# Optimization experiments

Hardware: AMD Instinct MI355X
Metric: run time of the kernel (lower is better)

## Reference

```python
import jax, jax.numpy as jnp
import numpy as np

NUM_HEADS = 4
KEY_DIM = 128


def rel_to_abs(rel):
    # rel: [B, heads, L, ww, 2*ww-1] -> [B, heads, L, ww, ww]
    B, heads, L, ww, dim = rel.shape
    flat = rel.reshape(B, heads, L, ww * (2 * ww - 1))[:, :, :, ww - 1:-1]
    return flat.reshape(B, heads, L, ww, 2 * (ww - 1))[..., :ww]


def relative_logits(pos_q, pos_emb_w, pos_emb_h):
    # pos_q: [B, hh, ww, heads, kd]
    # width logits
    q_w = jnp.transpose(pos_q, (0, 3, 1, 2, 4))           # [B, heads, hh, ww, kd]
    rel_w = jnp.einsum('bhxyd,dr->bhxyr', q_w, pos_emb_w)  # [B, heads, hh, ww, 2ww-1]
    rel_w = rel_to_abs(rel_w)                              # [B, heads, hh, ww, ww]
    # height logits
    q_h = jnp.transpose(pos_q, (0, 3, 2, 1, 4))           # [B, heads, ww, hh, kd]
    rel_h = jnp.einsum('bhyxd,dr->bhyxr', q_h, pos_emb_h)  # [B, heads, ww, hh, 2hh-1]
    rel_h = rel_to_abs(rel_h)                              # [B, heads, ww, hh, hh]
    rel_h = jnp.transpose(rel_h, (0, 1, 3, 2, 4))          # [B, heads, hh, ww, hh]
    # broadcast-add: [B, heads, hh, ww, hh, ww]
    return rel_w[:, :, :, :, None, :] + rel_h[:, :, :, :, :, None]


def setup_inputs() -> dict:
    key = jax.random.key(0)
    ks = jax.random.split(key, 7)
    B, H, W, C = 8, 32, 32, 512
    emb = NUM_HEADS * KEY_DIM
    stddev = KEY_DIM ** (-0.5)
    return {
        'x': jax.random.normal(ks[0], (B, H, W, C), jnp.float32),
        'Wq': jax.random.normal(ks[1], (C, emb), jnp.float32) * 0.02,
        'Wk': jax.random.normal(ks[2], (C, emb), jnp.float32) * 0.02,
        'Wv': jax.random.normal(ks[3], (C, emb), jnp.float32) * 0.02,
        'Wo': jax.random.normal(ks[4], (emb, emb), jnp.float32) * 0.02,
        'pos_emb_w': jax.random.normal(ks[5], (KEY_DIM, 2 * W - 1), jnp.float32) * stddev,
        'pos_emb_h': jax.random.normal(ks[6], (KEY_DIM, 2 * H - 1), jnp.float32) * stddev,
    }


def reference(x, Wq, Wk, Wv, Wo, pos_emb_w, pos_emb_h):
    B, hh, ww, C = x.shape
    heads, kd = NUM_HEADS, KEY_DIM
    L = hh * ww
    scale = 1.0 / jnp.sqrt(jnp.asarray(kd, x.dtype))

    q = (x @ Wq) * scale                                    # [B, hh, ww, heads*kd]
    attn_q = q.reshape(B, L, heads, kd).transpose(0, 2, 1, 3)   # [B, heads, L, kd]
    pos_q = q.reshape(B, hh, ww, heads, kd)
    k = (x @ Wk).reshape(B, L, heads, kd).transpose(0, 2, 3, 1)  # [B, heads, kd, L]
    v = (x @ Wv).reshape(B, L, heads, kd).transpose(0, 2, 1, 3)  # [B, heads, L, kd]

    scores = attn_q @ k                                      # [B, heads, L, L]
    pos = relative_logits(pos_q, pos_emb_w, pos_emb_h)        # [B, heads, hh, ww, hh, ww]
    scores = scores + pos.reshape(B, heads, L, L)
    attn = jax.nn.softmax(scores, axis=-1)

    out = attn @ v                                            # [B, heads, L, kd]
    out = out.transpose(0, 2, 1, 3).reshape(B, hh, ww, heads * kd)
    return out @ Wo
```

## Files before the change

kernel.cpp:

```cpp
#include <hip/hip_runtime.h>
#include <math.h>

typedef unsigned short u16;
typedef unsigned int u32;
typedef __bf16 bf16x8 __attribute__((ext_vector_type(8)));
typedef float f32x4 __attribute__((ext_vector_type(4)));

__device__ __forceinline__ u16 f2b(float f) {
  u32 u = __builtin_bit_cast(u32, f);
  u32 r = (u + 0x7FFFu + ((u >> 16) & 1u)) >> 16;
  return (u16)r;
}

__device__ __forceinline__ void glds16(const void* g, void* lds) {
  __builtin_amdgcn_global_load_lds(
      (const __attribute__((address_space(1))) void*)(void*)(const_cast<void*>(g)),
      (__attribute__((address_space(3))) void*)lds, 16, 0, 0);
}

#define QSCALE (0.08838834764831845f * 1.4426950408889634f)


__global__ __launch_bounds__(256) void castx(const float* __restrict__ x, u16* __restrict__ xb) {
  int idx = blockIdx.x * 256 + threadIdx.x;
  float4 v = ((const float4*)x)[idx];
  ushort4 o;
  o.x = f2b(v.x); o.y = f2b(v.y); o.z = f2b(v.z); o.w = f2b(v.w);
  ((ushort4*)xb)[idx] = o;
}

__global__ __launch_bounds__(256) void buildw(const float* __restrict__ Wq, const float* __restrict__ Wk,
                                              const float* __restrict__ Wv, const float* __restrict__ Wo,
                                              u16* __restrict__ WbigT, u16* __restrict__ WoT) {
  int row = blockIdx.x;
  int t = threadIdx.x;
  if (row < 512) {
    for (int k = t; k < 512; k += 256) WbigT[row*512 + k] = f2b(Wq[k*512 + row] * QSCALE);
  } else if (row < 1024) {
    int n = row - 512;
    for (int k = t; k < 512; k += 256) WbigT[row*512 + k] = f2b(Wk[k*512 + n]);
  } else if (row < 1536) {
    int n = row - 1024;
    for (int k = t; k < 512; k += 256) WbigT[row*512 + k] = f2b(Wv[k*512 + n]);
  } else if (row < 1544) {
    int rr = row - 1536 + 2040;
    for (int k = t; k < 512; k += 256) WbigT[rr*512 + k] = 0;
  } else {
    int n = row - 1544;
    for (int k = t; k < 512; k += 256) WoT[n*512 + k] = f2b(Wo[k*512 + n]);
  }
}

__global__ __launch_bounds__(256) void wpe_kernel(const float* __restrict__ Wq, const float* __restrict__ pew,
                                                  const float* __restrict__ peh, u16* __restrict__ WbigT) {
  int k = blockIdx.x;
  int t = threadIdx.x;
  __shared__ float wrow[512];
  for (int j = t; j < 512; j += 256) wrow[j] = Wq[k*512 + j];
  __syncthreads();
  if (t < 252) {
    int h = t / 63, r = t - h*63;
    float aw = 0.f, ah = 0.f;
    for (int d = 0; d < 128; d++) {
      float qv = wrow[h*128 + d];
      aw += qv * pew[d*63 + r];
      ah += qv * peh[d*63 + r];
    }
    WbigT[(size_t)(1536 + t)*512 + k] = f2b(aw * QSCALE);
    WbigT[(size_t)(1788 + t)*512 + k] = f2b(ah * QSCALE);
  }
}

__global__ __launch_bounds__(512) void gemm256(
    const u16* __restrict__ A, const u16* __restrict__ Bt,
    u16* __restrict__ Qb, u16* __restrict__ Kb, u16* __restrict__ Vt,
    float* __restrict__ RELW, float* __restrict__ RELH)
{
  __shared__ char sm[131072];
  const int tid = threadIdx.x;
  const int w = tid >> 6, l = tid & 63, g = l >> 4, c = l & 15;
  const int bm = blockIdx.x, bn = blockIdx.y;
  const int wm = w >> 2, wn = w & 3;

  f32x4 acc[8][4];
#pragma unroll
  for (int i = 0; i < 8; i++)
#pragma unroll
    for (int j = 0; j < 4; j++) acc[i][j] = f32x4{0.f, 0.f, 0.f, 0.f};

  const char* Ab = (const char*)A;
  const char* Bb = (const char*)Bt;
  const int rsub = l >> 3;
  const int csw = (((l & 7) ^ rsub) << 4);

#define A_STAGE(kb, p)                                                                    \
  {                                                                                       \
    char* As_ = sm + (p)*65536;                                                           \
    const int kbyte = (kb) * 128;                                                         \
    _Pragma("unroll")                                                                     \
    for (int i2 = 0; i2 < 4; i2++) {                                                      \
      const int row = i2*64 + w*8 + rsub;                                                 \
      glds16(Ab + (size_t)(bm*256 + row) * 1024 + kbyte + csw, As_ + i2*8192 + w*1024);   \
    }                                                                                     \
  }
#define B_STAGE(kb, p)                                                                    \
  {                                                                                       \
    char* Bs_ = sm + (p)*65536 + 32768;                                                   \
    const int kbyte = (kb) * 128;                                                         \
    _Pragma("unroll")                                                                     \
    for (int i2 = 0; i2 < 4; i2++) {                                                      \
      const int row = i2*64 + w*8 + rsub;                                                 \
      glds16(Bb + (size_t)(bn*256 + row) * 1024 + kbyte + csw, Bs_ + i2*8192 + w*1024);   \
    }                                                                                     \
  }

  B_STAGE(0, 0); A_STAGE(0, 0);
  B_STAGE(1, 1); A_STAGE(1, 1);

#pragma unroll
  for (int kb = 0; kb < 8; kb++) {
    const int p = kb & 1;
    if (kb == 0)      { asm volatile("s_waitcnt vmcnt(8)" ::: "memory"); }
    else if (kb < 7)  { asm volatile("s_waitcnt vmcnt(4)" ::: "memory"); }
    else              { asm volatile("s_waitcnt vmcnt(0)" ::: "memory"); }
    __builtin_amdgcn_s_barrier();

    const char* As_ = sm + p*65536;
    const char* Bs_ = As_ + 32768;

    bf16x8 bf[4][2], af[4][2];
#pragma unroll
    for (int ks = 0; ks < 2; ks++) {
      const int koff = (ks*64 + g*16) ^ ((c & 7) << 4);
#pragma unroll
      for (int mf = 0; mf < 4; mf++)
        af[mf][ks] = *(const bf16x8*)(As_ + (wm*128 + mf*16 + c)*128 + koff);
#pragma unroll
      for (int nf = 0; nf < 4; nf++)
        bf[nf][ks] = *(const bf16x8*)(Bs_ + (wn*64 + nf*16 + c)*128 + koff);
    }
    if (kb >= 1 && kb < 7) A_STAGE(kb + 1, p ^ 1);
    __builtin_amdgcn_s_setprio(1);
#pragma unroll
    for (int ks = 0; ks < 2; ks++)
#pragma unroll
      for (int mf = 0; mf < 4; mf++)
#pragma unroll
        for (int nf = 0; nf < 4; nf++)
          acc[mf][nf] = __builtin_amdgcn_mfma_f32_16x16x32_bf16(af[mf][ks], bf[nf][ks], acc[mf][nf], 0, 0, 0);
    __builtin_amdgcn_s_setprio(0);
    __builtin_amdgcn_s_barrier();

#pragma unroll
    for (int ks = 0; ks < 2; ks++) {
      const int koff = (ks*64 + g*16) ^ ((c & 7) << 4);
#pragma unroll
      for (int mf = 0; mf < 4; mf++)
        af[mf][ks] = *(const bf16x8*)(As_ + (wm*128 + (mf + 4)*16 + c)*128 + koff);
    }
    if (kb < 6) B_STAGE(kb + 2, p);
    __builtin_amdgcn_s_setprio(1);
#pragma unroll
    for (int ks = 0; ks < 2; ks++)
#pragma unroll
      for (int mf = 0; mf < 4; mf++)
#pragma unroll
        for (int nf = 0; nf < 4; nf++)
          acc[mf + 4][nf] = __builtin_amdgcn_mfma_f32_16x16x32_bf16(af[mf][ks], bf[nf][ks], acc[mf + 4][nf], 0, 0, 0);
    __builtin_amdgcn_s_setprio(0);
    __builtin_amdgcn_s_barrier();
  }
#undef A_STAGE
#undef B_STAGE

  const int b = bm >> 2;
  const int iBase = (bm & 3) * 256;

  if (bn < 4) {
    u16* dst0 = (bn < 2) ? Qb : Kb;
    const int bnn = bn & 1;
#pragma unroll
    for (int mf = 0; mf < 8; mf++) {
      const int lmb = wm*128 + mf*16 + g*4;
#pragma unroll
      for (int nf = 0; nf < 4; nf++) {
        const int ln = wn*64 + nf*16 + c;
#pragma unroll
        for (int r = 0; r < 4; r++) {
          const int lm = lmb + r;
          *(u16*)(sm + lm*512 + ((ln*2) ^ ((lm & 7) << 4))) = f2b(acc[mf][nf][r]);
        }
      }
    }
    __builtin_amdgcn_s_barrier();
#pragma unroll
    for (int it = 0; it < 16; it++) {
      const int gid = it*512 + tid;
      const int lm2 = gid >> 5, gsub = gid & 31;
      bf16x8 v = *(const bf16x8*)(sm + lm2*512 + ((gsub*16) ^ ((lm2 & 7) << 4)));
      const int h = bnn*2 + (gsub >> 4);
      const int d0 = (gsub & 15) * 8;
      *(bf16x8*)(dst0 + ((size_t)(b*4 + h)*1024 + iBase + lm2)*128 + d0) = v;
    }
  } else if (bn < 6) {
#pragma unroll
    for (int mf = 0; mf < 8; mf++) {
      const int lmb = wm*128 + mf*16 + g*4;
#pragma unroll
      for (int nf = 0; nf < 4; nf++) {
        const int ln = wn*64 + nf*16 + c;
        u32 w0, w1;
        asm("v_cvt_pk_bf16_f32 %0, %1, %2" : "=v"(w0) : "v"(acc[mf][nf][0]), "v"(acc[mf][nf][1]));
        asm("v_cvt_pk_bf16_f32 %0, %1, %2" : "=v"(w1) : "v"(acc[mf][nf][2]), "v"(acc[mf][nf][3]));
        uint2 pk; pk.x = w0; pk.y = w1;
        *(uint2*)(sm + ln*512 + ((lmb*2) ^ ((c & 7) << 4))) = pk;
      }
    }
    __builtin_amdgcn_s_barrier();
#pragma unroll
    for (int it = 0; it < 16; it++) {
      const int gid = it*512 + tid;
      const int ln2 = gid >> 5, gsub = gid & 31;
      bf16x8 v = *(const bf16x8*)(sm + ln2*512 + ((gsub*16) ^ ((ln2 & 7) << 4)));
      const int q2 = (bn - 4)*256 + ln2;
      const int h = q2 >> 7, d = q2 & 127;
      *(bf16x8*)(Vt + ((size_t)(b*4 + h)*128 + d)*1024 + iBase + gsub*8) = v;
    }
  } else {
#pragma unroll
    for (int mf = 0; mf < 8; mf++) {
      const int lmb = wm*128 + mf*16 + g*4;
#pragma unroll
      for (int nf = 0; nf < 4; nf++) {
        const int q = (bn - 6)*256 + wn*64 + nf*16 + c;
        if (q < 252) {
          const int h = q / 63, r2 = q - h*63;
#pragma unroll
          for (int r = 0; r < 4; r++)
            RELW[(size_t)((b*4 + h)*1024 + iBase + lmb + r)*64 + r2] = acc[mf][nf][r];
        } else if (q < 504) {
          const int qq = q - 252;
          const int h = qq / 63, r2 = qq - h*63;
#pragma unroll
          for (int r = 0; r < 4; r++)
            RELH[(size_t)((b*4 + h)*1024 + iBase + lmb + r)*64 + r2] = acc[mf][nf][r];
        }
      }
    }
  }
}

__global__ __launch_bounds__(256) void attn_fused(
    const u16* __restrict__ Qb, const u16* __restrict__ Kb, const u16* __restrict__ Vt,
    const float* __restrict__ RELW, const float* __restrict__ RELH,
    u16* __restrict__ AO)
{
  __shared__ char sm[73728];
  char* const Pl = sm + 65536;
  const int tid = threadIdx.x;
  const int w = tid >> 6, l = tid & 63, g = l >> 4, c = l & 15;
  const int bh = blockIdx.x, qt = blockIdx.y;
  const int i0 = qt * 64;

  bf16x8 qf[4];
  {
    const char* qbase = (const char*)Qb + (size_t)(bh*1024 + i0 + w*16 + c) * 256;
#pragma unroll
    for (int s = 0; s < 4; s++) qf[s] = *(const bf16x8*)(qbase + s*64 + g*16);
  }

  const int i = i0 + w*16 + c;
  const int xi = i & 31, yi = i >> 5;
  const float* rw = RELW + ((size_t)(bh*1024 + i) << 6);
  const float* rhb = RELH + ((size_t)(bh*1024 + i) << 6) + (31 - yi);
  float xwh[2][4];
#pragma unroll
  for (int e = 0; e < 2; e++)
#pragma unroll
    for (int r = 0; r < 4; r++) xwh[e][r] = rw[e*16 + g*4 + r - xi + 31];

  f32x4 Oacc[8];
#pragma unroll
  for (int fd = 0; fd < 8; fd++) Oacc[fd] = f32x4{0.f, 0.f, 0.f, 0.f};
  float m_q = -INFINITY, l_q = 0.f;

#define A_STAGE(jt, p)                                                                     \
  {                                                                                        \
    char* Kt_ = sm + (p)*32768;                                                            \
    char* Vs_ = Kt_ + 16384;                                                               \
    const int j0b = (jt) * 64;                                                             \
    _Pragma("unroll")                                                                      \
    for (int t = 0; t < 4; t++) {                                                          \
      const int L = (w*4 + t)*1024 + l*16;                                                 \
      const int jr = L >> 8, jb = L & 255;                                                 \
      glds16((const char*)Kb + (size_t)(bh*1024 + j0b + jr) * 256 + (jb ^ ((jr & 7) << 4)),\
             Kt_ + L);                                                                     \
      const int dr = L >> 7, db = L & 127;                                                 \
      glds16((const char*)Vt + (size_t)(bh*128 + dr) * 2048 + j0b*2 + (db ^ ((dr & 7) << 4)),\
             Vs_ + L);                                                                     \
    }                                                                                      \
  }

  A_STAGE(0, 0);
  A_STAGE(1, 1);
  float yh0 = rhb[0], yh1 = rhb[1];

#pragma unroll 2
  for (int jt = 0; jt < 16; jt++) {
    const int p = jt & 1;
    if (jt < 15) { asm volatile("s_waitcnt vmcnt(8)" ::: "memory"); }
    else         { asm volatile("s_waitcnt vmcnt(0)" ::: "memory"); }
    __builtin_amdgcn_s_barrier();

    const char* Kt_ = sm + p*32768;
    const char* Vs_ = Kt_ + 16384;

    f32x4 acc[4];
#pragma unroll
    for (int fn = 0; fn < 4; fn++) acc[fn] = f32x4{0.f, 0.f, 0.f, 0.f};
    __builtin_amdgcn_s_setprio(1);
#pragma unroll
    for (int s = 0; s < 4; s++) {
      const int koff = (s*64 + g*16) ^ ((c & 7) << 4);
#pragma unroll
      for (int fn = 0; fn < 4; fn++) {
        bf16x8 kf = *(const bf16x8*)(Kt_ + (fn*16 + c)*256 + koff);
        acc[fn] = __builtin_amdgcn_mfma_f32_16x16x32_bf16(kf, qf[s], acc[fn], 0, 0, 0);
      }
    }
    __builtin_amdgcn_s_setprio(0);

#pragma unroll
    for (int fn = 0; fn < 4; fn++)
#pragma unroll
      for (int r = 0; r < 4; r++)
        acc[fn][r] += xwh[fn & 1][r] + ((fn >> 1) ? yh1 : yh0);

    float mx = fmaxf(fmaxf(fmaxf(acc[0][0], acc[0][1]), fmaxf(acc[0][2], acc[0][3])),
                     fmaxf(fmaxf(acc[1][0], acc[1][1]), fmaxf(acc[1][2], acc[1][3])));
    mx = fmaxf(mx, fmaxf(fmaxf(fmaxf(acc[2][0], acc[2][1]), fmaxf(acc[2][2], acc[2][3])),
                         fmaxf(fmaxf(acc[3][0], acc[3][1]), fmaxf(acc[3][2], acc[3][3]))));
    mx = fmaxf(mx, __shfl_xor(mx, 16));
    mx = fmaxf(mx, __shfl_xor(mx, 32));

    if (__any(mx > m_q + 8.f)) {
      const float mnew = fmaxf(m_q, mx);
      const float scq = exp2f(m_q - mnew);
      m_q = mnew;
      l_q *= scq;
#pragma unroll
      for (int r = 0; r < 4; r++) {
        const float scr = __shfl(scq, g*4 + r, 16);
#pragma unroll
        for (int fd = 0; fd < 8; fd++) Oacc[fd][r] *= scr;
      }
    }

    float pv[4][4];
    float ps = 0.f;
#pragma unroll
    for (int fn = 0; fn < 4; fn++) {
#pragma unroll
      for (int r = 0; r < 4; r++) {
        pv[fn][r] = exp2f(acc[fn][r] - m_q);
        ps += pv[fn][r];
      }
    }
    ps += __shfl_xor(ps, 16);
    ps += __shfl_xor(ps, 32);
    l_q += ps;

    float nyh0 = 0.f, nyh1 = 0.f;
    if (jt < 15) { nyh0 = rhb[(jt + 1)*2]; nyh1 = rhb[(jt + 1)*2 + 1]; }

    {
      char* pb = Pl + w*2048 + c*128;
      const int swz = (c & 7) << 4;
#pragma unroll
      for (int fn = 0; fn < 4; fn++) {
        u32 w0, w1;
        asm("v_cvt_pk_bf16_f32 %0, %1, %2" : "=v"(w0) : "v"(pv[fn][0]), "v"(pv[fn][1]));
        asm("v_cvt_pk_bf16_f32 %0, %1, %2" : "=v"(w1) : "v"(pv[fn][2]), "v"(pv[fn][3]));
        uint2 pk; pk.x = w0; pk.y = w1;
        *(uint2*)(pb + ((fn*32 + g*8) ^ swz)) = pk;
      }
    }

    __builtin_amdgcn_s_setprio(1);
#pragma unroll
    for (int s = 0; s < 2; s++) {
      const int koff = (s*64 + g*16) ^ ((c & 7) << 4);
      bf16x8 pf = *(const bf16x8*)(Pl + w*2048 + c*128 + koff);
#pragma unroll
      for (int fd = 0; fd < 8; fd++) {
        bf16x8 vf = *(const bf16x8*)(Vs_ + (fd*16 + c)*128 + koff);
        Oacc[fd] = __builtin_amdgcn_mfma_f32_16x16x32_bf16(pf, vf, Oacc[fd], 0, 0, 0);
      }
    }
    __builtin_amdgcn_s_setprio(0);

    __builtin_amdgcn_s_barrier();
    if (jt < 14) A_STAGE(jt + 2, p);
    yh0 = nyh0; yh1 = nyh1;
  }

  const int b = bh >> 2, h = bh & 3;
#pragma unroll
  for (int r = 0; r < 4; r++) {
    const float lr = __shfl(l_q, g*4 + r, 16);
    const float linv = 1.0f / lr;
    const int io = i0 + w*16 + g*4 + r;
#pragma unroll
    for (int fd = 0; fd < 8; fd++) {
      AO[(size_t)(b*1024 + io)*512 + h*128 + fd*16 + c] = f2b(Oacc[fd][r] * linv);
    }
  }
#undef A_STAGE
}

__global__ __launch_bounds__(256) void gemm_out(
    const u16* __restrict__ A, const u16* __restrict__ Bt, float* __restrict__ outF)
{
  __shared__ char sm[65536];
  const int tid = threadIdx.x;
  const int w = tid >> 6, l = tid & 63, g = l >> 4, c = l & 15;
  const int bm = blockIdx.x, bn = blockIdx.y;
  const int wm = (w >> 1) * 64, wn = (w & 1) * 64;

  f32x4 acc[4][4];
#pragma unroll
  for (int i = 0; i < 4; i++)
#pragma unroll
    for (int j = 0; j < 4; j++) acc[i][j] = f32x4{0.f, 0.f, 0.f, 0.f};

  const char* Ab = (const char*)A;
  const char* Bb = (const char*)Bt;
  const int rsub = l >> 3;
  const int csw = (((l & 7) ^ rsub) << 4);

#define G_STAGE(kb, p)                                                                    \
  {                                                                                       \
    char* As_ = sm + (p)*32768;                                                           \
    char* Bs_ = As_ + 16384;                                                              \
    const int kbyte = (kb) * 128;                                                         \
    _Pragma("unroll")                                                                     \
    for (int t = 0; t < 4; t++) {                                                         \
      const int row = (w*4 + t)*8 + rsub;                                                 \
      glds16(Ab + (size_t)(bm*128 + row) * 1024 + kbyte + csw, As_ + (w*4 + t)*1024);     \
      glds16(Bb + (size_t)(bn*128 + row) * 1024 + kbyte + csw, Bs_ + (w*4 + t)*1024);     \
    }                                                                                     \
  }

  G_STAGE(0, 0);
  G_STAGE(1, 1);

#pragma unroll
  for (int kb = 0; kb < 8; kb++) {
    const int p = kb & 1;
    if (kb < 7) { asm volatile("s_waitcnt vmcnt(8)" ::: "memory"); }
    else        { asm volatile("s_waitcnt vmcnt(0)" ::: "memory"); }
    __builtin_amdgcn_s_barrier();
    const char* As_ = sm + p*32768;
    const char* Bs_ = As_ + 16384;
#pragma unroll
    for (int ks = 0; ks < 2; ks++) {
      const int koff = (ks*64 + g*16) ^ ((c & 7) << 4);
      bf16x8 af[4], bfr[4];
#pragma unroll
      for (int mf = 0; mf < 4; mf++)
        af[mf] = *(const bf16x8*)(As_ + (wm + mf*16 + c)*128 + koff);
#pragma unroll
      for (int nf = 0; nf < 4; nf++)
        bfr[nf] = *(const bf16x8*)(Bs_ + (wn + nf*16 + c)*128 + koff);
#pragma unroll
      for (int mf = 0; mf < 4; mf++)
#pragma unroll
        for (int nf = 0; nf < 4; nf++)
          acc[mf][nf] = __builtin_amdgcn_mfma_f32_16x16x32_bf16(af[mf], bfr[nf], acc[mf][nf], 0, 0, 0);
    }
    __builtin_amdgcn_s_barrier();
    if (kb < 6) G_STAGE(kb + 2, p);
  }
#undef G_STAGE

#pragma unroll
  for (int mf = 0; mf < 4; mf++) {
#pragma unroll
    for (int nf = 0; nf < 4; nf++) {
      const int n = bn*128 + wn + nf*16 + c;
#pragma unroll
      for (int r = 0; r < 4; r++) {
        const int m = bm*128 + wm + mf*16 + g*4 + r;
        outF[(size_t)m*512 + n] = acc[mf][nf][r];
      }
    }
  }
}

extern "C" void kernel_launch(void* const* d_in, const int* in_sizes, int n_in,
                              void* d_out, int out_size, void* d_ws, size_t ws_size,
                              hipStream_t stream) {
  const float* x   = (const float*)d_in[0];
  const float* Wq  = (const float*)d_in[1];
  const float* Wk  = (const float*)d_in[2];
  const float* Wv  = (const float*)d_in[3];
  const float* Wo  = (const float*)d_in[4];
  const float* pew = (const float*)d_in[5];
  const float* peh = (const float*)d_in[6];

  char* ws = (char*)d_ws;
  u16* xb    = (u16*)ws;    ws += (size_t)8192*512*2;
  u16* WbigT = (u16*)ws;    ws += (size_t)2048*512*2;
  u16* WoT   = (u16*)ws;    ws += (size_t)512*512*2;
  u16* Qb    = (u16*)ws;    ws += (size_t)32*1024*128*2;
  u16* Kb    = (u16*)ws;    ws += (size_t)32*1024*128*2;
  u16* Vt    = (u16*)ws;    ws += (size_t)32*1024*128*2;
  float* RELW = (float*)ws; ws += (size_t)32*1024*64*4;
  float* RELH = (float*)ws; ws += (size_t)32*1024*64*4;
  u16* AO    = (u16*)ws;    ws += (size_t)8192*512*2;

  castx<<<4096, 256, 0, stream>>>(x, xb);
  buildw<<<2056, 256, 0, stream>>>(Wq, Wk, Wv, Wo, WbigT, WoT);
  wpe_kernel<<<512, 256, 0, stream>>>(Wq, pew, peh, WbigT);
  gemm256<<<dim3(32, 8), 512, 0, stream>>>(xb, WbigT, Qb, Kb, Vt, RELW, RELH);
  attn_fused<<<dim3(32, 16), 256, 0, stream>>>(Qb, Kb, Vt, RELW, RELH, AO);
  gemm_out<<<dim3(64, 4), 256, 0, stream>>>(AO, WoT, (float*)d_out);
}
```

Measured before the change: 97.55 us.

## Software-pipeline QK^T one tile ahead and merge prep kernels into one launch

The attention kernel now stages K and V tiles separately and computes the QK^T MFMAs for tile jt+1 while tile jt's softmax and PV run, double-buffering the score accumulators. The goal is to hide softmax latency behind matrix work and to issue K loads earlier. It also merges the three preprocessing kernels (x cast, weight transpose, positional-weight fold) into one launch to cut launch overhead. The price is more live registers for the second accumulator set, which may reduce occupancy, plus more delicate vmcnt accounting.

```diff
diff --git a/kernel.cpp b/kernel.cpp
--- a/kernel.cpp
+++ b/kernel.cpp
@@ -20,54 +20,53 @@
 
 #define QSCALE (0.08838834764831845f * 1.4426950408889634f)
 
-
-__global__ __launch_bounds__(256) void castx(const float* __restrict__ x, u16* __restrict__ xb) {
-  int idx = blockIdx.x * 256 + threadIdx.x;
-  float4 v = ((const float4*)x)[idx];
-  ushort4 o;
-  o.x = f2b(v.x); o.y = f2b(v.y); o.z = f2b(v.z); o.w = f2b(v.w);
-  ((ushort4*)xb)[idx] = o;
-}
-
-__global__ __launch_bounds__(256) void buildw(const float* __restrict__ Wq, const float* __restrict__ Wk,
-                                              const float* __restrict__ Wv, const float* __restrict__ Wo,
-                                              u16* __restrict__ WbigT, u16* __restrict__ WoT) {
-  int row = blockIdx.x;
-  int t = threadIdx.x;
-  if (row < 512) {
-    for (int k = t; k < 512; k += 256) WbigT[row*512 + k] = f2b(Wq[k*512 + row] * QSCALE);
-  } else if (row < 1024) {
-    int n = row - 512;
-    for (int k = t; k < 512; k += 256) WbigT[row*512 + k] = f2b(Wk[k*512 + n]);
-  } else if (row < 1536) {
-    int n = row - 1024;
-    for (int k = t; k < 512; k += 256) WbigT[row*512 + k] = f2b(Wv[k*512 + n]);
-  } else if (row < 1544) {
-    int rr = row - 1536 + 2040;
-    for (int k = t; k < 512; k += 256) WbigT[rr*512 + k] = 0;
+__global__ __launch_bounds__(256) void prep_all(
+    const float* __restrict__ x, const float* __restrict__ Wq, const float* __restrict__ Wk,
+    const float* __restrict__ Wv, const float* __restrict__ Wo,
+    const float* __restrict__ pew, const float* __restrict__ peh,
+    u16* __restrict__ xb, u16* __restrict__ WbigT, u16* __restrict__ WoT)
+{
+  __shared__ float wrow[512];
+  const int bid = blockIdx.x;
+  const int t = threadIdx.x;
+  if (bid < 4096) {
+    int idx = bid * 256 + t;
+    float4 v = ((const float4*)x)[idx];
+    ushort4 o;
+    o.x = f2b(v.x); o.y = f2b(v.y); o.z = f2b(v.z); o.w = f2b(v.w);
+    ((ushort4*)xb)[idx] = o;
+  } else if (bid < 6152) {
+    int row = bid - 4096;
+    if (row < 512) {
+      for (int k = t; k < 512; k += 256) WbigT[row*512 + k] = f2b(Wq[k*512 + row] * QSCALE);
+    } else if (row < 1024) {
+      int n = row - 512;
+      for (int k = t; k < 512; k += 256) WbigT[row*512 + k] = f2b(Wk[k*512 + n]);
+    } else if (row < 1536) {
+      int n = row - 1024;
+      for (int k = t; k < 512; k += 256) WbigT[row*512 + k] = f2b(Wv[k*512 + n]);
+    } else if (row < 1544) {
+      int rr = row - 1536 + 2040;
+      for (int k = t; k < 512; k += 256) WbigT[rr*512 + k] = 0;
+    } else {
+      int n = row - 1544;
+      for (int k = t; k < 512; k += 256) WoT[n*512 + k] = f2b(Wo[k*512 + n]);
+    }
   } else {
-    int n = row - 1544;
-    for (int k = t; k < 512; k += 256) WoT[n*512 + k] = f2b(Wo[k*512 + n]);
-  }
-}
-
-__global__ __launch_bounds__(256) void wpe_kernel(const float* __restrict__ Wq, const float* __restrict__ pew,
-                                                  const float* __restrict__ peh, u16* __restrict__ WbigT) {
-  int k = blockIdx.x;
-  int t = threadIdx.x;
-  __shared__ float wrow[512];
-  for (int j = t; j < 512; j += 256) wrow[j] = Wq[k*512 + j];
-  __syncthreads();
-  if (t < 252) {
-    int h = t / 63, r = t - h*63;
-    float aw = 0.f, ah = 0.f;
-    for (int d = 0; d < 128; d++) {
-      float qv = wrow[h*128 + d];
-      aw += qv * pew[d*63 + r];
-      ah += qv * peh[d*63 + r];
-    }
-    WbigT[(size_t)(1536 + t)*512 + k] = f2b(aw * QSCALE);
-    WbigT[(size_t)(1788 + t)*512 + k] = f2b(ah * QSCALE);
+    int k = bid - 6152;
+    for (int j = t; j < 512; j += 256) wrow[j] = Wq[k*512 + j];
+    __syncthreads();
+    if (t < 252) {
+      int h = t / 63, r = t - h*63;
+      float aw = 0.f, ah = 0.f;
+      for (int d = 0; d < 128; d++) {
+        float qv = wrow[h*128 + d];
+        aw += qv * pew[d*63 + r];
+        ah += qv * peh[d*63 + r];
+      }
+      WbigT[(size_t)(1536 + t)*512 + k] = f2b(aw * QSCALE);
+      WbigT[(size_t)(1788 + t)*512 + k] = f2b(ah * QSCALE);
+    }
   }
 }
 
@@ -279,15 +278,9 @@
 #pragma unroll
     for (int r = 0; r < 4; r++) xwh[e][r] = rw[e*16 + g*4 + r - xi + 31];
 
-  f32x4 Oacc[8];
-#pragma unroll
-  for (int fd = 0; fd < 8; fd++) Oacc[fd] = f32x4{0.f, 0.f, 0.f, 0.f};
-  float m_q = -INFINITY, l_q = 0.f;
-
-#define A_STAGE(jt, p)                                                                     \
+#define K_STAGE(jt, p)                                                                     \
   {                                                                                        \
-    char* Kt_ = sm + (p)*32768;                                                            \
-    char* Vs_ = Kt_ + 16384;                                                               \
+    char* Kt_ = sm + (p)*16384;                                                            \
     const int j0b = (jt) * 64;                                                             \
     _Pragma("unroll")                                                                      \
     for (int t = 0; t < 4; t++) {                                                          \
@@ -295,41 +288,65 @@
       const int jr = L >> 8, jb = L & 255;                                                 \
       glds16((const char*)Kb + (size_t)(bh*1024 + j0b + jr) * 256 + (jb ^ ((jr & 7) << 4)),\
              Kt_ + L);                                                                     \
+    }                                                                                      \
+  }
+#define V_STAGE(jt, p)                                                                     \
+  {                                                                                        \
+    char* Vs_ = sm + 32768 + (p)*16384;                                                    \
+    const int j0b = (jt) * 64;                                                             \
+    _Pragma("unroll")                                                                      \
+    for (int t = 0; t < 4; t++) {                                                          \
+      const int L = (w*4 + t)*1024 + l*16;                                                 \
       const int dr = L >> 7, db = L & 127;                                                 \
       glds16((const char*)Vt + (size_t)(bh*128 + dr) * 2048 + j0b*2 + (db ^ ((dr & 7) << 4)),\
              Vs_ + L);                                                                     \
     }                                                                                      \
   }
-
-  A_STAGE(0, 0);
-  A_STAGE(1, 1);
+#define QK_COMPUTE(jtX, accX)                                                              \
+  {                                                                                        \
+    const char* Kt_ = sm + ((jtX) & 1)*16384;                                              \
+    _Pragma("unroll")                                                                      \
+    for (int fn = 0; fn < 4; fn++) (accX)[fn] = f32x4{0.f, 0.f, 0.f, 0.f};                 \
+    __builtin_amdgcn_s_setprio(1);                                                         \
+    _Pragma("unroll")                                                                      \
+    for (int s = 0; s < 4; s++) {                                                          \
+      const int koff = (s*64 + g*16) ^ ((c & 7) << 4);                                     \
+      _Pragma("unroll")                                                                    \
+      for (int fn = 0; fn < 4; fn++) {                                                     \
+        bf16x8 kf = *(const bf16x8*)(Kt_ + (fn*16 + c)*256 + koff);                        \
+        (accX)[fn] = __builtin_amdgcn_mfma_f32_16x16x32_bf16(kf, qf[s], (accX)[fn], 0, 0, 0);\
+      }                                                                                    \
+    }                                                                                      \
+    __builtin_amdgcn_s_setprio(0);                                                         \
+  }
+
+  f32x4 Oacc[8];
+#pragma unroll
+  for (int fd = 0; fd < 8; fd++) Oacc[fd] = f32x4{0.f, 0.f, 0.f, 0.f};
+  float m_q = -INFINITY, l_q = 0.f;
+  f32x4 acc2[2][4];
+
   float yh0 = rhb[0], yh1 = rhb[1];
+  asm volatile("" ::: "memory");
+  K_STAGE(0, 0);
+  K_STAGE(1, 1);
+  V_STAGE(0, 0);
+  V_STAGE(1, 1);
+  asm volatile("s_waitcnt vmcnt(12)" ::: "memory");
+  __builtin_amdgcn_s_barrier();
+  QK_COMPUTE(0, acc2[0]);
 
 #pragma unroll 2
   for (int jt = 0; jt < 16; jt++) {
     const int p = jt & 1;
-    if (jt < 15) { asm volatile("s_waitcnt vmcnt(8)" ::: "memory"); }
+    if (jt < 15) { asm volatile("s_waitcnt vmcnt(4)" ::: "memory"); }
     else         { asm volatile("s_waitcnt vmcnt(0)" ::: "memory"); }
     __builtin_amdgcn_s_barrier();
 
-    const char* Kt_ = sm + p*32768;
-    const char* Vs_ = Kt_ + 16384;
-
-    f32x4 acc[4];
-#pragma unroll
-    for (int fn = 0; fn < 4; fn++) acc[fn] = f32x4{0.f, 0.f, 0.f, 0.f};
-    __builtin_amdgcn_s_setprio(1);
-#pragma unroll
-    for (int s = 0; s < 4; s++) {
-      const int koff = (s*64 + g*16) ^ ((c & 7) << 4);
-#pragma unroll
-      for (int fn = 0; fn < 4; fn++) {
-        bf16x8 kf = *(const bf16x8*)(Kt_ + (fn*16 + c)*256 + koff);
-        acc[fn] = __builtin_amdgcn_mfma_f32_16x16x32_bf16(kf, qf[s], acc[fn], 0, 0, 0);
-      }
-    }
-    __builtin_amdgcn_s_setprio(0);
-
+    if (jt < 14) K_STAGE(jt + 2, p);
+    if (jt < 15) QK_COMPUTE(jt + 1, acc2[(jt + 1) & 1]);
+
+    f32x4* acc = acc2[p];
 #pragma unroll
     for (int fn = 0; fn < 4; fn++)
 #pragma unroll
@@ -387,22 +404,28 @@
     }
 
     __builtin_amdgcn_s_setprio(1);
-#pragma unroll
-    for (int s = 0; s < 2; s++) {
-      const int koff = (s*64 + g*16) ^ ((c & 7) << 4);
-      bf16x8 pf = *(const bf16x8*)(Pl + w*2048 + c*128 + koff);
-#pragma unroll
-      for (int fd = 0; fd < 8; fd++) {
-        bf16x8 vf = *(const bf16x8*)(Vs_ + (fd*16 + c)*128 + koff);
-        Oacc[fd] = __builtin_amdgcn_mfma_f32_16x16x32_bf16(pf, vf, Oacc[fd], 0, 0, 0);
+    {
+      const char* Vs_ = sm + 32768 + p*16384;
+#pragma unroll
+      for (int s = 0; s < 2; s++) {
+        const int koff = (s*64 + g*16) ^ ((c & 7) << 4);
+        bf16x8 pf = *(const bf16x8*)(Pl + w*2048 + c*128 + koff);
+#pragma unroll
+        for (int fd = 0; fd < 8; fd++) {
+          bf16x8 vf = *(const bf16x8*)(Vs_ + (fd*16 + c)*128 + koff);
+          Oacc[fd] = __builtin_amdgcn_mfma_f32_16x16x32_bf16(pf, vf, Oacc[fd], 0, 0, 0);
+        }
       }
     }
     __builtin_amdgcn_s_setprio(0);
 
     __builtin_amdgcn_s_barrier();
-    if (jt < 14) A_STAGE(jt + 2, p);
+    if (jt < 14) V_STAGE(jt + 2, p);
     yh0 = nyh0; yh1 = nyh1;
   }
+#undef K_STAGE
+#undef V_STAGE
+#undef QK_COMPUTE
 
   const int b = bh >> 2, h = bh & 3;
 #pragma unroll
@@ -415,7 +438,6 @@
       AO[(size_t)(b*1024 + io)*512 + h*128 + fd*16 + c] = f2b(Oacc[fd][r] * linv);
     }
   }
-#undef A_STAGE
 }
 
 __global__ __launch_bounds__(256) void gemm_out(
@@ -519,9 +541,7 @@
   float* RELH = (float*)ws; ws += (size_t)32*1024*64*4;
   u16* AO    = (u16*)ws;    ws += (size_t)8192*512*2;
 
-  castx<<<4096, 256, 0, stream>>>(x, xb);
-  buildw<<<2056, 256, 0, stream>>>(Wq, Wk, Wv, Wo, WbigT, WoT);
-  wpe_kernel<<<512, 256, 0, stream>>>(Wq, pew, peh, WbigT);
+  prep_all<<<6664, 256, 0, stream>>>(x, Wq, Wk, Wv, Wo, pew, peh, xb, WbigT, WoT);
   gemm256<<<dim3(32, 8), 512, 0, stream>>>(xb, WbigT, Qb, Kb, Vt, RELW, RELH);
   attn_fused<<<dim3(32, 16), 256, 0, stream>>>(Qb, Kb, Vt, RELW, RELH, AO);
   gemm_out<<<dim3(64, 4), 256, 0, stream>>>(AO, WoT, (float*)d_out);
```

Measured after the change: 101.1 us. 1.04x slower.

## Merge prep kernels and enlarge attention query tile to 128 rows

Applied to the files above, without the earlier changes.

Folds the three preprocessing kernels (x cast, weight transpose, positional-weight fold) into one launch to cut launch overhead. The attention kernel now uses 512 threads per block covering 128 queries, so each K/V tile staged in LDS is reused by twice as many waves. Each thread issues half as many async loads, and the wait count is adjusted to match. This halves the grid to 256 blocks, which could hurt occupancy or latency hiding on a GPU with many CUs, and raises LDS use per block.

```diff
diff --git a/kernel.cpp b/kernel.cpp
--- a/kernel.cpp
+++ b/kernel.cpp
@@ -20,54 +20,53 @@
 
 #define QSCALE (0.08838834764831845f * 1.4426950408889634f)
 
-
-__global__ __launch_bounds__(256) void castx(const float* __restrict__ x, u16* __restrict__ xb) {
-  int idx = blockIdx.x * 256 + threadIdx.x;
-  float4 v = ((const float4*)x)[idx];
-  ushort4 o;
-  o.x = f2b(v.x); o.y = f2b(v.y); o.z = f2b(v.z); o.w = f2b(v.w);
-  ((ushort4*)xb)[idx] = o;
-}
-
-__global__ __launch_bounds__(256) void buildw(const float* __restrict__ Wq, const float* __restrict__ Wk,
-                                              const float* __restrict__ Wv, const float* __restrict__ Wo,
-                                              u16* __restrict__ WbigT, u16* __restrict__ WoT) {
-  int row = blockIdx.x;
-  int t = threadIdx.x;
-  if (row < 512) {
-    for (int k = t; k < 512; k += 256) WbigT[row*512 + k] = f2b(Wq[k*512 + row] * QSCALE);
-  } else if (row < 1024) {
-    int n = row - 512;
-    for (int k = t; k < 512; k += 256) WbigT[row*512 + k] = f2b(Wk[k*512 + n]);
-  } else if (row < 1536) {
-    int n = row - 1024;
-    for (int k = t; k < 512; k += 256) WbigT[row*512 + k] = f2b(Wv[k*512 + n]);
-  } else if (row < 1544) {
-    int rr = row - 1536 + 2040;
-    for (int k = t; k < 512; k += 256) WbigT[rr*512 + k] = 0;
+__global__ __launch_bounds__(256) void prep_all(
+    const float* __restrict__ x, const float* __restrict__ Wq, const float* __restrict__ Wk,
+    const float* __restrict__ Wv, const float* __restrict__ Wo,
+    const float* __restrict__ pew, const float* __restrict__ peh,
+    u16* __restrict__ xb, u16* __restrict__ WbigT, u16* __restrict__ WoT)
+{
+  __shared__ float wrow[512];
+  const int bid = blockIdx.x;
+  const int t = threadIdx.x;
+  if (bid < 4096) {
+    int idx = bid * 256 + t;
+    float4 v = ((const float4*)x)[idx];
+    ushort4 o;
+    o.x = f2b(v.x); o.y = f2b(v.y); o.z = f2b(v.z); o.w = f2b(v.w);
+    ((ushort4*)xb)[idx] = o;
+  } else if (bid < 6152) {
+    int row = bid - 4096;
+    if (row < 512) {
+      for (int k = t; k < 512; k += 256) WbigT[row*512 + k] = f2b(Wq[k*512 + row] * QSCALE);
+    } else if (row < 1024) {
+      int n = row - 512;
+      for (int k = t; k < 512; k += 256) WbigT[row*512 + k] = f2b(Wk[k*512 + n]);
+    } else if (row < 1536) {
+      int n = row - 1024;
+      for (int k = t; k < 512; k += 256) WbigT[row*512 + k] = f2b(Wv[k*512 + n]);
+    } else if (row < 1544) {
+      int rr = row - 1536 + 2040;
+      for (int k = t; k < 512; k += 256) WbigT[rr*512 + k] = 0;
+    } else {
+      int n = row - 1544;
+      for (int k = t; k < 512; k += 256) WoT[n*512 + k] = f2b(Wo[k*512 + n]);
+    }
   } else {
-    int n = row - 1544;
-    for (int k = t; k < 512; k += 256) WoT[n*512 + k] = f2b(Wo[k*512 + n]);
-  }
-}
-
-__global__ __launch_bounds__(256) void wpe_kernel(const float* __restrict__ Wq, const float* __restrict__ pew,
-                                                  const float* __restrict__ peh, u16* __restrict__ WbigT) {
-  int k = blockIdx.x;
-  int t = threadIdx.x;
-  __shared__ float wrow[512];
-  for (int j = t; j < 512; j += 256) wrow[j] = Wq[k*512 + j];
-  __syncthreads();
-  if (t < 252) {
-    int h = t / 63, r = t - h*63;
-    float aw = 0.f, ah = 0.f;
-    for (int d = 0; d < 128; d++) {
-      float qv = wrow[h*128 + d];
-      aw += qv * pew[d*63 + r];
-      ah += qv * peh[d*63 + r];
-    }
-    WbigT[(size_t)(1536 + t)*512 + k] = f2b(aw * QSCALE);
-    WbigT[(size_t)(1788 + t)*512 + k] = f2b(ah * QSCALE);
+    int k = bid - 6152;
+    for (int j = t; j < 512; j += 256) wrow[j] = Wq[k*512 + j];
+    __syncthreads();
+    if (t < 252) {
+      int h = t / 63, r = t - h*63;
+      float aw = 0.f, ah = 0.f;
+      for (int d = 0; d < 128; d++) {
+        float qv = wrow[h*128 + d];
+        aw += qv * pew[d*63 + r];
+        ah += qv * peh[d*63 + r];
+      }
+      WbigT[(size_t)(1536 + t)*512 + k] = f2b(aw * QSCALE);
+      WbigT[(size_t)(1788 + t)*512 + k] = f2b(ah * QSCALE);
+    }
   }
 }
 
@@ -250,17 +249,17 @@
   }
 }
 
-__global__ __launch_bounds__(256) void attn_fused(
+__global__ __launch_bounds__(512) void attn_fused(
     const u16* __restrict__ Qb, const u16* __restrict__ Kb, const u16* __restrict__ Vt,
     const float* __restrict__ RELW, const float* __restrict__ RELH,
     u16* __restrict__ AO)
 {
-  __shared__ char sm[73728];
+  __shared__ char sm[81920];
   char* const Pl = sm + 65536;
   const int tid = threadIdx.x;
   const int w = tid >> 6, l = tid & 63, g = l >> 4, c = l & 15;
   const int bh = blockIdx.x, qt = blockIdx.y;
-  const int i0 = qt * 64;
+  const int i0 = qt * 128;
 
   bf16x8 qf[4];
   {
@@ -286,12 +285,12 @@
 
 #define A_STAGE(jt, p)                                                                     \
   {                                                                                        \
-    char* Kt_ = sm + (p)*32768;                                                            \
-    char* Vs_ = Kt_ + 16384;                                                               \
+    char* Kt_ = sm + (p)*16384;                                                            \
+    char* Vs_ = sm + 32768 + (p)*16384;                                                    \
     const int j0b = (jt) * 64;                                                             \
     _Pragma("unroll")                                                                      \
-    for (int t = 0; t < 4; t++) {                                                          \
-      const int L = (w*4 + t)*1024 + l*16;                                                 \
+    for (int t = 0; t < 2; t++) {                                                          \
+      const int L = (w*2 + t)*1024 + l*16;                                                 \
       const int jr = L >> 8, jb = L & 255;                                                 \
       glds16((const char*)Kb + (size_t)(bh*1024 + j0b + jr) * 256 + (jb ^ ((jr & 7) << 4)),\
              Kt_ + L);                                                                     \
@@ -301,19 +300,20 @@
     }                                                                                      \
   }
 
+  float yh0 = rhb[0], yh1 = rhb[1];
+  asm volatile("" ::: "memory");
   A_STAGE(0, 0);
   A_STAGE(1, 1);
-  float yh0 = rhb[0], yh1 = rhb[1];
 
 #pragma unroll 2
   for (int jt = 0; jt < 16; jt++) {
     const int p = jt & 1;
-    if (jt < 15) { asm volatile("s_waitcnt vmcnt(8)" ::: "memory"); }
+    if (jt < 15) { asm volatile("s_waitcnt vmcnt(4)" ::: "memory"); }
     else         { asm volatile("s_waitcnt vmcnt(0)" ::: "memory"); }
     __builtin_amdgcn_s_barrier();
 
-    const char* Kt_ = sm + p*32768;
-    const char* Vs_ = Kt_ + 16384;
+    const char* Kt_ = sm + p*16384;
+    const char* Vs_ = sm + 32768 + p*16384;
 
     f32x4 acc[4];
 #pragma unroll
@@ -403,6 +403,7 @@
     if (jt < 14) A_STAGE(jt + 2, p);
     yh0 = nyh0; yh1 = nyh1;
   }
+#undef A_STAGE
 
   const int b = bh >> 2, h = bh & 3;
 #pragma unroll
@@ -415,7 +416,6 @@
       AO[(size_t)(b*1024 + io)*512 + h*128 + fd*16 + c] = f2b(Oacc[fd][r] * linv);
     }
   }
-#undef A_STAGE
 }
 
 __global__ __launch_bounds__(256) void gemm_out(
@@ -519,10 +519,8 @@
   float* RELH = (float*)ws; ws += (size_t)32*1024*64*4;
   u16* AO    = (u16*)ws;    ws += (size_t)8192*512*2;
 
-  castx<<<4096, 256, 0, stream>>>(x, xb);
-  buildw<<<2056, 256, 0, stream>>>(Wq, Wk, Wv, Wo, WbigT, WoT);
-  wpe_kernel<<<512, 256, 0, stream>>>(Wq, pew, peh, WbigT);
+  prep_all<<<6664, 256, 0, stream>>>(x, Wq, Wk, Wv, Wo, pew, peh, xb, WbigT, WoT);
   gemm256<<<dim3(32, 8), 512, 0, stream>>>(xb, WbigT, Qb, Kb, Vt, RELW, RELH);
-  attn_fused<<<dim3(32, 16), 256, 0, stream>>>(Qb, Kb, Vt, RELW, RELH, AO);
+  attn_fused<<<dim3(32, 8), 512, 0, stream>>>(Qb, Kb, Vt, RELW, RELH, AO);
   gemm_out<<<dim3(64, 4), 256, 0, stream>>>(AO, WoT, (float*)d_out);
 }
```

New measurement: 97.42 us. About the same (-0.1%).
